# Kernel optimization log

Measured on AMD Instinct MI355X. Metric: run time of the kernel, lower is better.

The kernel has to match this reference:

```python
import jax, jax.numpy as jnp
import numpy as np
from jax import lax

NQ, DEPTH = 4, 2

# ---- tiny state-vector simulator helpers (2^NQ = 16 amplitudes) ----

def _c(t):
    return t.astype(jnp.complex64)

def _rx(t):
    c, s = _c(jnp.cos(t / 2)), _c(jnp.sin(t / 2))
    return jnp.stack([jnp.stack([c, -1j * s]), jnp.stack([-1j * s, c])])

def _ry(t):
    c, s = _c(jnp.cos(t / 2)), _c(jnp.sin(t / 2))
    return jnp.stack([jnp.stack([c, -s]), jnp.stack([s, c])])

def _rz(t):
    e = jnp.exp(-1j * _c(t) / 2)
    z = jnp.zeros((), jnp.complex64)
    return jnp.stack([jnp.stack([e, z]), jnp.stack([z, jnp.conj(e)])])

def _apply_1q(state, U, w):
    st = jnp.tensordot(U, state, axes=((1,), (w,)))
    return jnp.moveaxis(st, 0, w)

_CNOT = np.array([[1, 0, 0, 0], [0, 1, 0, 0], [0, 0, 0, 1], [0, 0, 1, 0]], dtype=np.complex64)

def _apply_cnot(state, w):
    st = jnp.moveaxis(state, (w, w + 1), (0, 1))
    shp = st.shape
    st = jnp.asarray(_CNOT) @ st.reshape(4, -1)
    return jnp.moveaxis(st.reshape(shp), (0, 1), (w, w + 1))

def quantum_expvals(q_params, q_basis):
    # |0...0> initial state, shape (2,)*NQ
    state = jnp.zeros((2,) * NQ, jnp.complex64).at[(0,) * NQ].set(1.0)
    for w in range(NQ):  # learnable basis rotation
        state = _apply_1q(state, _rx(q_basis[w, 0]), w)
        state = _apply_1q(state, _ry(q_basis[w, 1]), w)
        state = _apply_1q(state, _rz(q_basis[w, 2]), w)
    for layer in range(DEPTH):
        for w in range(NQ):
            state = _apply_1q(state, _rx(q_params[layer, w, 0]), w)
            state = _apply_1q(state, _ry(q_params[layer, w, 1]), w)
            state = _apply_1q(state, _rz(q_params[layer, w, 2]), w)
        for w in range(NQ - 1):
            state = _apply_cnot(state, w)
    probs = jnp.abs(state) ** 2  # real, (2,)*NQ
    z = jnp.array([1.0, -1.0], jnp.float32)
    evs = [jnp.tensordot(probs.sum(axis=tuple(i for i in range(NQ) if i != w)), z, 1) for w in range(NQ)]
    return jnp.stack(evs)  # [NQ]


def _maxpool_2x2_s1(x):
    return lax.reduce_window(x, -jnp.inf, lax.max, (1, 1, 2, 2), (1, 1, 1, 1), 'VALID')


def setup_inputs() -> dict:
    key = jax.random.key(0)
    ks = jax.random.split(key, 14)
    B = 1024
    g = lambda k, shp, s=0.02: (jax.random.normal(k, shp, jnp.float32) * s)
    return {
        'x': jax.random.normal(ks[0], (B, 3, 66, 66), jnp.float32),
        'conv1_w': g(ks[1], (8, 3, 5, 5), 0.05), 'conv1_b': g(ks[2], (8,)),
        'conv2_w': g(ks[3], (16, 8, 3, 3), 0.05), 'conv2_b': g(ks[4], (16,)),
        'fc1_w': g(ks[5], (120, 16 * 15 * 15)), 'fc1_b': g(ks[6], (120,)),
        'fc2_w': g(ks[7], (84, 120)), 'fc2_b': g(ks[8], (84,)),
        'q_params': jax.random.normal(ks[9], (DEPTH, NQ, 3), jnp.float32),
        'q_basis': jax.random.normal(ks[10], (NQ, 3), jnp.float32),
        'fc3_w': g(ks[11], (1, NQ)), 'fc3_b': g(ks[12], (1,)),
    }


def reference(x, conv1_w, conv1_b, conv2_w, conv2_b, fc1_w, fc1_b, fc2_w, fc2_b, q_params, q_basis, fc3_w, fc3_b):
    dn = ('NCHW', 'OIHW', 'NCHW')
    h = lax.conv_general_dilated(x, conv1_w, (2, 2), ((1, 1), (1, 1)), dimension_numbers=dn)
    h = jax.nn.relu(h + conv1_b[None, :, None, None])  # [B,8,32,32]
    h = _maxpool_2x2_s1(h)  # [B,8,31,31] (dropout = identity in eval)
    h = lax.conv_general_dilated(h, conv2_w, (2, 2), ((1, 1), (1, 1)), dimension_numbers=dn)
    h = jax.nn.relu(h + conv2_b[None, :, None, None])  # [B,16,16,16]
    h = _maxpool_2x2_s1(h)  # [B,16,15,15]
    h = h.reshape(h.shape[0], -1)  # [B,3600]
    h = jax.nn.relu(h @ fc1_w.T + fc1_b)
    h = jax.nn.relu(h @ fc2_w.T + fc2_b)  # [B,84] (quantum circuit ignores these features)
    evs = quantum_expvals(q_params, q_basis)  # [NQ], identical for every sample
    quantum_out = jnp.broadcast_to(evs, (h.shape[0], NQ))
    logits = quantum_out @ fc3_w.T + fc3_b  # [B,1]
    probs = jax.nn.sigmoid(logits)[:, 0]
    return jnp.stack([probs, 1.0 - probs], axis=-1)  # [B,2]
```

## Files before the change

### kernel.cpp

```cpp
#include <hip/hip_runtime.h>
#include <math.h>


struct c32 { float x, y; };

__device__ __forceinline__ void apply1q(c32* a, int mask,
                                        c32 u00, c32 u01, c32 u10, c32 u11) {
#pragma unroll
    for (int s = 0; s < 16; ++s) {
        if (s & mask) continue;
        c32 a0 = a[s];
        c32 a1 = a[s | mask];
        c32 n0, n1;
        n0.x = u00.x * a0.x - u00.y * a0.y + u01.x * a1.x - u01.y * a1.y;
        n0.y = u00.x * a0.y + u00.y * a0.x + u01.x * a1.y + u01.y * a1.x;
        n1.x = u10.x * a0.x - u10.y * a0.y + u11.x * a1.x - u11.y * a1.y;
        n1.y = u10.x * a0.y + u10.y * a0.x + u11.x * a1.y + u11.y * a1.x;
        a[s] = n0;
        a[s | mask] = n1;
    }
}

__device__ __forceinline__ void rot3(c32* a, int w, float tx, float ty, float tz) {
    const int mask = 8 >> w;
    float sx, cx, sy, cy, sz, cz;
    sincosf(0.5f * tx, &sx, &cx);
    apply1q(a, mask, {cx, 0.f}, {0.f, -sx}, {0.f, -sx}, {cx, 0.f});
    sincosf(0.5f * ty, &sy, &cy);
    apply1q(a, mask, {cy, 0.f}, {-sy, 0.f}, {sy, 0.f}, {cy, 0.f});
    sincosf(0.5f * tz, &sz, &cz);
    apply1q(a, mask, {cz, -sz}, {0.f, 0.f}, {0.f, 0.f}, {cz, sz});
}

__device__ __forceinline__ void cnot(c32* a, int w) {
    const int cm = 8 >> w;
    const int tm = 8 >> (w + 1);
#pragma unroll
    for (int s = 0; s < 16; ++s) {
        if ((s & cm) && !(s & tm)) {
            c32 t = a[s];
            a[s] = a[s | tm];
            a[s | tm] = t;
        }
    }
}

__global__ void __launch_bounds__(256)
qhbc_kernel(const float* __restrict__ q_params,
            const float* __restrict__ q_basis,
            const float* __restrict__ fc3_w,
            const float* __restrict__ fc3_b,
            float* __restrict__ out,
            int n_rows) {
    c32 a[16];
#pragma unroll
    for (int i = 0; i < 16; ++i) a[i] = {0.f, 0.f};
    a[0] = {1.f, 0.f};

#pragma unroll
    for (int w = 0; w < 4; ++w)
        rot3(a, w, q_basis[w * 3 + 0], q_basis[w * 3 + 1], q_basis[w * 3 + 2]);

#pragma unroll
    for (int l = 0; l < 2; ++l) {
#pragma unroll
        for (int w = 0; w < 4; ++w) {
            const int base = (l * 4 + w) * 3;
            rot3(a, w, q_params[base + 0], q_params[base + 1], q_params[base + 2]);
        }
#pragma unroll
        for (int w = 0; w < 3; ++w) cnot(a, w);
    }

    float ev0 = 0.f, ev1 = 0.f, ev2 = 0.f, ev3 = 0.f;
#pragma unroll
    for (int s = 0; s < 16; ++s) {
        const float p = a[s].x * a[s].x + a[s].y * a[s].y;
        ev0 += (s & 8) ? -p : p;
        ev1 += (s & 4) ? -p : p;
        ev2 += (s & 2) ? -p : p;
        ev3 += (s & 1) ? -p : p;
    }

    const float logit = ev0 * fc3_w[0] + ev1 * fc3_w[1] + ev2 * fc3_w[2] +
                        ev3 * fc3_w[3] + fc3_b[0];
    const float p = 1.f / (1.f + expf(-logit));

    const int i = blockIdx.x * blockDim.x + threadIdx.x;
    if (i < n_rows) {
        float2* o = reinterpret_cast<float2*>(out);
        o[i] = make_float2(p, 1.f - p);
    }
}

extern "C" void kernel_launch(void* const* d_in, const int* in_sizes, int n_in,
                              void* d_out, int out_size, void* d_ws, size_t ws_size,
                              hipStream_t stream) {
    const float* q_params = (const float*)d_in[9];
    const float* q_basis  = (const float*)d_in[10];
    const float* fc3_w    = (const float*)d_in[11];
    const float* fc3_b    = (const float*)d_in[12];
    float* out = (float*)d_out;

    const int n_rows = out_size / 2;
    const int block = 256;
    const int grid = (n_rows + block - 1) / block;
    qhbc_kernel<<<grid, block, 0, stream>>>(q_params, q_basis, fc3_w, fc3_b, out, n_rows);
}
```

Baseline: 111.2 us.

## Distribute state-vector amplitudes across lanes with shuffles and write float4 outputs

Rewrites the quantum simulation so each group of 16 lanes holds one amplitude per lane and applies gates through cross-lane xor shuffles, instead of every thread simulating all 16 amplitudes in registers. Expectation values are summed with a shuffle butterfly. Each thread now writes two output rows as one float4, which halves the thread count. This is meant to cut per-thread arithmetic and register pressure, at the cost of many shuffle operations and a dependence on out_size being divisible by 4.

```diff
diff --git a/kernel.cpp b/kernel.cpp
--- a/kernel.cpp
+++ b/kernel.cpp
@@ -2,47 +2,8 @@
 #include <math.h>
 
 
-struct c32 { float x, y; };
-
-__device__ __forceinline__ void apply1q(c32* a, int mask,
-                                        c32 u00, c32 u01, c32 u10, c32 u11) {
-#pragma unroll
-    for (int s = 0; s < 16; ++s) {
-        if (s & mask) continue;
-        c32 a0 = a[s];
-        c32 a1 = a[s | mask];
-        c32 n0, n1;
-        n0.x = u00.x * a0.x - u00.y * a0.y + u01.x * a1.x - u01.y * a1.y;
-        n0.y = u00.x * a0.y + u00.y * a0.x + u01.x * a1.y + u01.y * a1.x;
-        n1.x = u10.x * a0.x - u10.y * a0.y + u11.x * a1.x - u11.y * a1.y;
-        n1.y = u10.x * a0.y + u10.y * a0.x + u11.x * a1.y + u11.y * a1.x;
-        a[s] = n0;
-        a[s | mask] = n1;
-    }
-}
-
-__device__ __forceinline__ void rot3(c32* a, int w, float tx, float ty, float tz) {
-    const int mask = 8 >> w;
-    float sx, cx, sy, cy, sz, cz;
-    sincosf(0.5f * tx, &sx, &cx);
-    apply1q(a, mask, {cx, 0.f}, {0.f, -sx}, {0.f, -sx}, {cx, 0.f});
-    sincosf(0.5f * ty, &sy, &cy);
-    apply1q(a, mask, {cy, 0.f}, {-sy, 0.f}, {sy, 0.f}, {cy, 0.f});
-    sincosf(0.5f * tz, &sz, &cz);
-    apply1q(a, mask, {cz, -sz}, {0.f, 0.f}, {0.f, 0.f}, {cz, sz});
-}
-
-__device__ __forceinline__ void cnot(c32* a, int w) {
-    const int cm = 8 >> w;
-    const int tm = 8 >> (w + 1);
-#pragma unroll
-    for (int s = 0; s < 16; ++s) {
-        if ((s & cm) && !(s & tm)) {
-            c32 t = a[s];
-            a[s] = a[s | tm];
-            a[s | tm] = t;
-        }
-    }
+__device__ __forceinline__ float shx(float v, int m) {
+    return __shfl_xor(v, m, 64);
 }
 
 __global__ void __launch_bounds__(256)
@@ -50,47 +11,84 @@
             const float* __restrict__ q_basis,
             const float* __restrict__ fc3_w,
             const float* __restrict__ fc3_b,
-            float* __restrict__ out,
-            int n_rows) {
-    c32 a[16];
-#pragma unroll
-    for (int i = 0; i < 16; ++i) a[i] = {0.f, 0.f};
-    a[0] = {1.f, 0.f};
+            float4* __restrict__ out4,
+            int n4) {
+    const int lane = threadIdx.x & 63;
+
+    float ax = ((lane & 15) == 0) ? 1.f : 0.f;
+    float ay = 0.f;
+
+    auto RX = [&](int m, float t) {
+        float sn, cs; sincosf(0.5f * t, &sn, &cs);
+        float px = shx(ax, m), py = shx(ay, m);
+        float nx = cs * ax + sn * py;
+        float ny = cs * ay - sn * px;
+        ax = nx; ay = ny;
+    };
+    auto RY = [&](int m, float t) {
+        float sn, cs; sincosf(0.5f * t, &sn, &cs);
+        float px = shx(ax, m), py = shx(ay, m);
+        float ss = (lane & m) ? sn : -sn;
+        float nx = cs * ax + ss * px;
+        float ny = cs * ay + ss * py;
+        ax = nx; ay = ny;
+    };
+    auto RZ = [&](int m, float t) {
+        float sn, cs; sincosf(0.5f * t, &sn, &cs);
+        float sl = (lane & m) ? -sn : sn;
+        float nx = cs * ax + sl * ay;
+        float ny = cs * ay - sl * ax;
+        ax = nx; ay = ny;
+    };
+    auto CNOT = [&](int cm, int tm) {
+        float px = shx(ax, tm), py = shx(ay, tm);
+        const bool c = (lane & cm) != 0;
+        ax = c ? px : ax;
+        ay = c ? py : ay;
+    };
 
 #pragma unroll
-    for (int w = 0; w < 4; ++w)
-        rot3(a, w, q_basis[w * 3 + 0], q_basis[w * 3 + 1], q_basis[w * 3 + 2]);
+    for (int w = 0; w < 4; ++w) {
+        const int m = 8 >> w;
+        RX(m, q_basis[w * 3 + 0]);
+        RY(m, q_basis[w * 3 + 1]);
+        RZ(m, q_basis[w * 3 + 2]);
+    }
 
 #pragma unroll
     for (int l = 0; l < 2; ++l) {
 #pragma unroll
         for (int w = 0; w < 4; ++w) {
-            const int base = (l * 4 + w) * 3;
-            rot3(a, w, q_params[base + 0], q_params[base + 1], q_params[base + 2]);
+            const int m = 8 >> w;
+            const int b = (l * 4 + w) * 3;
+            RX(m, q_params[b + 0]);
+            RY(m, q_params[b + 1]);
+            RZ(m, q_params[b + 2]);
         }
-#pragma unroll
-        for (int w = 0; w < 3; ++w) cnot(a, w);
+        CNOT(8, 4);
+        CNOT(4, 2);
+        CNOT(2, 1);
     }
 
-    float ev0 = 0.f, ev1 = 0.f, ev2 = 0.f, ev3 = 0.f;
+    const float p = ax * ax + ay * ay;
+    float e0 = (lane & 8) ? -p : p;
+    float e1 = (lane & 4) ? -p : p;
+    float e2 = (lane & 2) ? -p : p;
+    float e3 = (lane & 1) ? -p : p;
 #pragma unroll
-    for (int s = 0; s < 16; ++s) {
-        const float p = a[s].x * a[s].x + a[s].y * a[s].y;
-        ev0 += (s & 8) ? -p : p;
-        ev1 += (s & 4) ? -p : p;
-        ev2 += (s & 2) ? -p : p;
-        ev3 += (s & 1) ? -p : p;
+    for (int m = 1; m < 16; m <<= 1) {
+        e0 += shx(e0, m);
+        e1 += shx(e1, m);
+        e2 += shx(e2, m);
+        e3 += shx(e3, m);
     }
 
-    const float logit = ev0 * fc3_w[0] + ev1 * fc3_w[1] + ev2 * fc3_w[2] +
-                        ev3 * fc3_w[3] + fc3_b[0];
-    const float p = 1.f / (1.f + expf(-logit));
+    const float logit = e0 * fc3_w[0] + e1 * fc3_w[1] + e2 * fc3_w[2] +
+                        e3 * fc3_w[3] + fc3_b[0];
+    const float pr = 1.f / (1.f + expf(-logit));
 
     const int i = blockIdx.x * blockDim.x + threadIdx.x;
-    if (i < n_rows) {
-        float2* o = reinterpret_cast<float2*>(out);
-        o[i] = make_float2(p, 1.f - p);
-    }
+    if (i < n4) out4[i] = make_float4(pr, 1.f - pr, pr, 1.f - pr);
 }
 
 extern "C" void kernel_launch(void* const* d_in, const int* in_sizes, int n_in,
@@ -100,10 +98,10 @@
     const float* q_basis  = (const float*)d_in[10];
     const float* fc3_w    = (const float*)d_in[11];
     const float* fc3_b    = (const float*)d_in[12];
-    float* out = (float*)d_out;
+    float4* out4 = (float4*)d_out;
 
-    const int n_rows = out_size / 2;
+    const int n4 = out_size / 4;
     const int block = 256;
-    const int grid = (n_rows + block - 1) / block;
-    qhbc_kernel<<<grid, block, 0, stream>>>(q_params, q_basis, fc3_w, fc3_b, out, n_rows);
+    const int grid = (n4 + block - 1) / block;
+    qhbc_kernel<<<grid, block, 0, stream>>>(q_params, q_basis, fc3_w, fc3_b, out4, n4);
 }
```

New measurement: 105.3 us. -5.3%, faster.
